# Optimization experiments

Hardware: AMD Instinct MI355X
Metric: run time of the kernel (lower is better)

## Reference

```python
import jax, jax.numpy as jnp
import numpy as np
from jax import lax

EPS = 1e-5

def _ln(x, w, b):
    m = jnp.mean(x, axis=-1, keepdims=True)
    v = jnp.mean((x - m) ** 2, axis=-1, keepdims=True)
    return (x - m) / jnp.sqrt(v + EPS) * w + b

def setup_inputs() -> dict:
    key = jax.random.key(0)
    ks = jax.random.split(key, 16)
    B, H, W, C = 4, 128, 128, 96
    N = H * W
    hidden = 192          # int(2.0 * dim)
    qk = 48               # dim // 2
    x = jax.random.normal(ks[0], (B, N, C), dtype=jnp.float32)
    # LayerNorm params
    norm_w = jnp.ones((C,), jnp.float32); norm_b = jnp.zeros((C,), jnp.float32)
    n1_w = jnp.ones((C,), jnp.float32); n1_b = jnp.zeros((C,), jnp.float32)
    n2_w = jnp.ones((C,), jnp.float32); n2_b = jnp.zeros((C,), jnp.float32)
    # Linear weights stored as [in, out]
    Wh = jax.random.normal(ks[1], (C, hidden), jnp.float32) * 0.02
    bh = jnp.zeros((hidden,), jnp.float32)
    Wqk = jax.random.normal(ks[2], (C, qk), jnp.float32) * 0.02
    bqk = jnp.zeros((qk,), jnp.float32)
    proj_w = jax.random.normal(ks[3], (C, C), jnp.float32) * 0.02
    proj_b = jnp.zeros((C,), jnp.float32)
    # per-branch affine on qk (init: normal std 0.02 / zeros, as in torch code)
    g1 = jax.random.normal(ks[4], (2, qk), jnp.float32) * 0.02
    be1 = jnp.zeros((2, qk), jnp.float32)
    g2 = jax.random.normal(ks[5], (2, qk), jnp.float32) * 0.02
    be2 = jnp.zeros((2, qk), jnp.float32)
    # SR convs (OIHW), kaiming-like init fan_out = k*k*C
    sr1_w = jax.random.normal(ks[6], (C, C, 8, 8), jnp.float32) * np.sqrt(2.0 / (8 * 8 * C))
    sr1_b = jnp.zeros((C,), jnp.float32)
    sr2_w = jax.random.normal(ks[7], (C, C, 4, 4), jnp.float32) * np.sqrt(2.0 / (4 * 4 * C))
    sr2_b = jnp.zeros((C,), jnp.float32)
    return dict(x=x, H=H, W=W, norm_w=norm_w, norm_b=norm_b, Wh=Wh, bh=bh,
                Wqk=Wqk, bqk=bqk, g1=g1, be1=be1, g2=g2, be2=be2,
                sr1_w=sr1_w, sr1_b=sr1_b, sr2_w=sr2_w, sr2_b=sr2_b,
                n1_w=n1_w, n1_b=n1_b, n2_w=n2_w, n2_b=n2_b,
                proj_w=proj_w, proj_b=proj_b)

def _sr_branch(xmap, cw, cb, lw, lb, stride):
    # xmap: [B,C,H,W]; strided conv with kernel==stride, then LN+GELU over tokens
    y = lax.conv_general_dilated(xmap, cw, (stride, stride), 'VALID',
                                 dimension_numbers=('NCHW', 'OIHW', 'NCHW'))
    y = y + cb[:, None, None]
    B, C = y.shape[0], y.shape[1]
    y = y.reshape(B, C, -1).transpose(0, 2, 1)  # [B, N', C]
    return jax.nn.gelu(_ln(y, lw, lb), approximate=False)

def reference(x, H, W, norm_w, norm_b, Wh, bh, Wqk, bqk, g1, be1, g2, be2,
              sr1_w, sr1_b, sr2_w, sr2_b, n1_w, n1_b, n2_w, n2_b, proj_w, proj_b):
    B, N, C = x.shape
    half = C // 2  # C // num_heads with num_heads=2
    nx = _ln(x, norm_w, norm_b)
    h = jax.nn.silu(nx @ Wh + bh)              # [B,N,2C]
    v, gate = h[..., :C], h[..., C:]
    xmap = nx.transpose(0, 2, 1).reshape(B, C, H, W)
    x1 = _sr_branch(xmap, sr1_w, sr1_b, n1_w, n1_b, 8)   # [B, N/64, C]
    x2 = _sr_branch(xmap, sr2_w, sr2_b, n2_w, n2_b, 4)   # [B, N/16, C]
    Z1 = jax.nn.silu(x1 @ Wqk + bqk)           # [B,N1,qk]
    QK1 = Z1[..., None, :] * g1 + be1          # [B,N1,2,qk]
    q1, k1 = QK1[..., 0, :], QK1[..., 1, :]
    Z2 = jax.nn.silu(x2 @ Wqk + bqk)
    QK2 = Z2[..., None, :] * g2 + be2
    q2, k2 = QK2[..., 0, :], QK2[..., 1, :]
    inv_n = 1.0 / N
    a1 = jnp.einsum('bnd,bmd->bnm', v[..., :half], q1) * inv_n
    A1 = jnp.square(jax.nn.relu(a1))
    V1 = jnp.einsum('bnm,bmd->bnd', A1, k1)
    a2 = jnp.einsum('bnd,bmd->bnm', v[..., half:], q2) * inv_n
    A2 = jnp.square(jax.nn.relu(a2))
    V2 = jnp.einsum('bnm,bmd->bnd', A2, k2)
    xc = jnp.concatenate([V1, V2], axis=-1)    # [B,N,C]
    value = xc * gate
    out = value @ proj_w + proj_b
    return out + xc
```

## Files before the change

kernel.cpp:

```cpp
#include <hip/hip_runtime.h>
#include <math.h>

#define NB   4
#define IH   128
#define IW   128
#define NTOK 16384
#define CC   96
#define HID  192
#define QKD  48
#define EPSF 1e-5f
#define INV_N (1.0f/16384.0f)

typedef __attribute__((ext_vector_type(8))) short sh8;
typedef __attribute__((ext_vector_type(4))) short ush4;
typedef __attribute__((ext_vector_type(4))) float f32x4;

__device__ __forceinline__ float wave_sum64(float v){
    #pragma unroll
    for (int off = 32; off > 0; off >>= 1) v += __shfl_xor(v, off, 64);
    return v;
}
__device__ __forceinline__ float siluf(float x){ return x / (1.0f + __expf(-x)); }
__device__ __forceinline__ float geluf(float x){ return 0.5f*x*(1.0f + erff(x*0.7071067811865475f)); }

__device__ __forceinline__ unsigned short f2bf(float f){
    union { float f; unsigned u; } x; x.f = f;
    unsigned u = x.u + 0x7FFFu + ((x.u >> 16) & 1u);
    return (unsigned short)(u >> 16);
}
__device__ __forceinline__ float b2f(unsigned hi16){
    union { unsigned u; float f; } c; c.u = hi16; return c.f;
}
__device__ __forceinline__ unsigned cvtpk(float a, float b){
    unsigned r;
    asm("v_cvt_pk_bf16_f32 %0, %1, %2" : "=v"(r) : "v"(a), "v"(b));
    return r;
}
__device__ __forceinline__ void swap32(unsigned &x, unsigned &y){
    asm volatile("v_permlane32_swap_b32 %0, %1" : "+v"(x), "+v"(y));
}
__device__ __forceinline__ void swap16(unsigned &x, unsigned &y){
    asm volatile("v_permlane16_swap_b32 %0, %1" : "+v"(x), "+v"(y));
}

__global__ __launch_bounds__(256) void k_ln(const float* __restrict__ x,
                                            const float* __restrict__ w,
                                            const float* __restrict__ bb,
                                            unsigned short* __restrict__ nxbf,
                                            unsigned short* __restrict__ nxim,
                                            const float* __restrict__ s1, unsigned short* __restrict__ d1, int n1,
                                            const float* __restrict__ s2, unsigned short* __restrict__ d2, int n2){
    int bid = blockIdx.x;
    if (bid >= 16384){
        int i4 = ((bid - 16384)*256 + threadIdx.x)*4;
        if (i4 < n1){
            float4 v = *(const float4*)(s1 + i4);
            unsigned u0 = cvtpk(v.x, v.y), u1 = cvtpk(v.z, v.w);
            ush4 o = {(short)u0, (short)(u0>>16), (short)u1, (short)(u1>>16)};
            *(ush4*)(d1 + i4) = o;
        } else {
            int j = i4 - n1;
            if (j < n2){
                float4 v = *(const float4*)(s2 + j);
                unsigned u0 = cvtpk(v.x, v.y), u1 = cvtpk(v.z, v.w);
                ush4 o = {(short)u0, (short)(u0>>16), (short)u1, (short)(u1>>16)};
                *(ush4*)(d2 + j) = o;
            }
        }
        return;
    }
    __shared__ unsigned short tile[4][96];
    int r = threadIdx.x >> 6;
    int row = bid*4 + r;
    int l = threadIdx.x & 63;
    const float* xr = x + (size_t)row*CC;
    float a = xr[l];
    float b = (l < 32) ? xr[64+l] : 0.0f;
    float s = wave_sum64(a + b);
    float m = s * (1.0f/96.0f);
    float d1f = a - m;
    float d2f = b - m;
    float sq = d1f*d1f + ((l < 32) ? d2f*d2f : 0.0f);
    float var = wave_sum64(sq) * (1.0f/96.0f);
    float rstd = rsqrtf(var + EPSF);
    unsigned short b1 = f2bf(d1f*rstd*w[l] + bb[l]);
    nxbf[(size_t)row*CC + l] = b1;
    tile[r][l] = b1;
    if (l < 32){
        unsigned short b2 = f2bf(d2f*rstd*w[64+l] + bb[64+l]);
        nxbf[(size_t)row*CC + 64 + l] = b2;
        tile[r][64+l] = b2;
    }
    __syncthreads();
    int t = threadIdx.x;
    if (t < 96){
        int row0 = bid*4;
        int bb2 = row0 >> 14, hw = row0 & 16383;
        ush4 v = {(short)tile[0][t], (short)tile[1][t], (short)tile[2][t], (short)tile[3][t]};
        *(ush4*)(nxim + (((size_t)(bb2*96 + t)) << 14) + hw) = v;
    }
}

__global__ __launch_bounds__(256) void k_hgemm(const unsigned short* __restrict__ nxbf,
                                               const float* __restrict__ Wh,
                                               const float* __restrict__ bh,
                                               unsigned short* __restrict__ vbuf,
                                               unsigned short* __restrict__ gate){
    __shared__ unsigned short whbf[192*100];
    int tid  = threadIdx.x;
    int lane = tid & 63;
    int wid  = tid >> 6;
    int lo   = lane & 15;
    int g    = lane >> 4;
    int row0 = blockIdx.x*64 + wid*16;

    #pragma unroll
    for (int it = 0; it < 36; it++){
        int pidx = tid + it*256;
        int k = pidx / 96, cp = (pidx - k*96)*2;
        float2 v = *(const float2*)&Wh[k*HID + cp];
        unsigned u = cvtpk(v.x, v.y);
        whbf[cp*100 + k]     = (unsigned short)u;
        whbf[(cp+1)*100 + k] = (unsigned short)(u >> 16);
    }

    sh8 a[3];
    {
        const unsigned short* ar = nxbf + (size_t)(row0 + lo)*CC;
        #pragma unroll
        for (int kc = 0; kc < 3; kc++)
            a[kc] = *(const sh8*)(ar + kc*32 + g*8);
    }
    __syncthreads();

    f32x4 acc[12];
    #pragma unroll
    for (int ct = 0; ct < 12; ct++) acc[ct] = (f32x4){0.f,0.f,0.f,0.f};
    #pragma unroll
    for (int ct = 0; ct < 12; ct++){
        #pragma unroll
        for (int kc = 0; kc < 3; kc++){
            sh8 bw = *(const sh8*)&whbf[(ct*16 + lo)*100 + kc*32 + g*8];
            acc[ct] = __builtin_amdgcn_mfma_f32_16x16x32_bf16(a[kc], bw, acc[ct], 0, 0, 0);
        }
    }

    #pragma unroll
    for (int ct = 0; ct < 12; ct++){
        int col = ct*16 + lo;
        float bcol = bh[col];
        #pragma unroll
        for (int j = 0; j < 4; j++){
            size_t row = row0 + g*4 + j;
            float hv = siluf(acc[ct][j] + bcol);
            unsigned short hb = (unsigned short)cvtpk(hv, hv);
            if (col < 96) vbuf[row*CC + col] = hb;
            else          gate[row*CC + col - 96] = hb;
        }
    }
}

__global__ __launch_bounds__(256) void k_conv(const unsigned short* __restrict__ nxim,
                                              const unsigned short* __restrict__ wbf,
                                              float* __restrict__ part,
                                              int posLog, int pdimLog, int pszLog,
                                              int kTotal, int rowblocks){
    __shared__ unsigned short pt[64*72];
    __shared__ unsigned short wt[96*72];
    int bx = blockIdx.x;
    int rb = bx % rowblocks;
    int split = bx / rowblocks;
    int tid = threadIdx.x;
    int lane = tid & 63, wid = tid >> 6, lo = lane & 15, g = lane >> 4;
    int psz = 1 << pszLog, pdim = 1 << pdimLog;
    int ksLog = 2*pszLog;
    int kb0 = split * 192;
    int cinc = (64 >> ksLog) << 14;

    int j   = tid & 15;
    int coff = (j*4) >> ksLog;
    int s   = (j*4) & (psz*psz - 1);
    int sy  = s >> pszLog, sx = s & (psz-1);
    int pAddr[4], pOff[4];
    #pragma unroll
    for (int i = 0; i < 4; i++){
        int p = (tid >> 4) + 16*i;
        int R = rb*64 + p;
        int b = R >> posLog, pp = R & ((1 << posLog) - 1);
        int pi = pp >> pdimLog, pj = pp & (pdim-1);
        pAddr[i] = (((b*96 + coff) + (kb0 >> ksLog)) << 14) + (pi*psz + sy)*IW + pj*psz + sx;
        pOff[i]  = p*72 + j*4;
    }
    int jj = tid & 7;
    int wAddr[3], wOff[3];
    #pragma unroll
    for (int i = 0; i < 3; i++){
        int o = (tid >> 3) + 32*i;
        wAddr[i] = o*kTotal + kb0 + jj*8;
        wOff[i]  = o*72 + jj*8;
    }

    f32x4 acc[6];
    #pragma unroll
    for (int ct = 0; ct < 6; ct++) acc[ct] = (f32x4){0.f,0.f,0.f,0.f};

    ush4 pr[4]; sh8 wr[3];
    #pragma unroll
    for (int i = 0; i < 4; i++) pr[i] = *(const ush4*)(nxim + pAddr[i]);
    #pragma unroll
    for (int i = 0; i < 3; i++) wr[i] = *(const sh8*)(wbf + wAddr[i]);

    for (int ch = 0; ch < 3; ch++){
        __syncthreads();
        #pragma unroll
        for (int i = 0; i < 4; i++) *(ush4*)&pt[pOff[i]] = pr[i];
        #pragma unroll
        for (int i = 0; i < 3; i++) *(sh8*)&wt[wOff[i]] = wr[i];
        if (ch < 2){
            #pragma unroll
            for (int i = 0; i < 4; i++){ pAddr[i] += cinc; pr[i] = *(const ush4*)(nxim + pAddr[i]); }
            #pragma unroll
            for (int i = 0; i < 3; i++){ wAddr[i] += 64;  wr[i] = *(const sh8*)(wbf + wAddr[i]); }
        }
        __syncthreads();

        sh8 a0 = *(const sh8*)&pt[(wid*16 + lo)*72 + g*8];
        sh8 a1 = *(const sh8*)&pt[(wid*16 + lo)*72 + 32 + g*8];
        #pragma unroll
        for (int ct = 0; ct < 6; ct++){
            sh8 b0 = *(const sh8*)&wt[(ct*16 + lo)*72 + g*8];
            sh8 b1 = *(const sh8*)&wt[(ct*16 + lo)*72 + 32 + g*8];
            acc[ct] = __builtin_amdgcn_mfma_f32_16x16x32_bf16(a0, b0, acc[ct], 0, 0, 0);
            acc[ct] = __builtin_amdgcn_mfma_f32_16x16x32_bf16(a1, b1, acc[ct], 0, 0, 0);
        }
    }

    int rowsTotal = NB << posLog;
    #pragma unroll
    for (int ct = 0; ct < 6; ct++){
        int o = ct*16 + lo;
        #pragma unroll
        for (int jx = 0; jx < 4; jx++){
            int R = rb*64 + wid*16 + g*4 + jx;
            part[((size_t)split*rowsTotal + R)*96 + o] = acc[ct][jx];
        }
    }
}

__global__ __launch_bounds__(64) void k_reduce(const float* __restrict__ part1,
                                               const float* __restrict__ part2,
                                               const float* __restrict__ cb1, const float* __restrict__ cb2,
                                               const float* __restrict__ lw1, const float* __restrict__ lw2,
                                               const float* __restrict__ lb1, const float* __restrict__ lb2,
                                               const float* __restrict__ wqk,
                                               const float* __restrict__ bqk,
                                               const float* __restrict__ g1, const float* __restrict__ g2,
                                               const float* __restrict__ be1, const float* __restrict__ be2,
                                               unsigned short* __restrict__ qp1, unsigned short* __restrict__ qp2,
                                               unsigned short* __restrict__ kt1, unsigned short* __restrict__ kt2){
    __shared__ float xsh[96];
    int bid = blockIdx.x;
    bool fst = bid < 1024;
    int row   = fst ? bid : bid - 1024;
    int nsplit= fst ? 32 : 8;
    int rows  = fst ? 1024 : 4096;
    int Mper  = fst ? 256 : 1024;
    const float* part = fst ? part1 : part2;
    const float* cbias= fst ? cb1 : cb2;
    const float* lw   = fst ? lw1 : lw2;
    const float* lb   = fst ? lb1 : lb2;
    const float* g    = fst ? g1 : g2;
    const float* be   = fst ? be1 : be2;
    unsigned short* qp = fst ? qp1 : qp2;
    unsigned short* ktp= fst ? kt1 : kt2;

    int l = threadIdx.x;
    float y1 = 0.0f, y2 = 0.0f;
    for (int s = 0; s < nsplit; s++){
        const float* pr = part + ((size_t)s*rows + row)*96;
        y1 += pr[l];
        if (l < 32) y2 += pr[64+l];
    }
    y1 += cbias[l];
    if (l < 32) y2 += cbias[64+l];
    float s = wave_sum64(y1 + ((l < 32) ? y2 : 0.0f));
    float m = s * (1.0f/96.0f);
    float d1 = y1 - m, d2 = y2 - m;
    float var = wave_sum64(d1*d1 + ((l < 32) ? d2*d2 : 0.0f)) * (1.0f/96.0f);
    float rstd = rsqrtf(var + EPSF);
    xsh[l] = geluf(d1*rstd*lw[l] + lb[l]);
    if (l < 32) xsh[64+l] = geluf(d2*rstd*lw[64+l] + lb[64+l]);
    __syncthreads();
    if (l < 48){
        float z = bqk[l];
        #pragma unroll 4
        for (int c = 0; c < 96; c++) z += xsh[c]*wqk[c*48 + l];
        z = siluf(z);
        float qv = (z*g[l]    + be[l]) * INV_N;
        float kv =  z*g[48+l] + be[48+l];
        int b = row / Mper, p = row - b*Mper;
        qp[(size_t)row*64 + l] = f2bf(qv);
        ktp[((size_t)b*48 + l)*Mper + p] = f2bf(kv);
    } else {
        qp[(size_t)row*64 + l] = 0;
    }
}

__global__ __launch_bounds__(256) void k_attn(const unsigned short* __restrict__ vbuf,
                                              const unsigned short* __restrict__ qp1,
                                              const unsigned short* __restrict__ ktp1,
                                              const unsigned short* __restrict__ qp2,
                                              const unsigned short* __restrict__ ktp2,
                                              unsigned short* __restrict__ V1,
                                              unsigned short* __restrict__ V2){
    __shared__ unsigned short qs[2][32*72];
    __shared__ unsigned short ks[2][48*72];

    int bx   = blockIdx.x;
    int kind = (bx < 512) ? 1 : 0;
    int blk  = (bx < 512) ? bx : bx - 512;
    int tid  = threadIdx.x;
    int wid  = tid >> 6;
    int lane = tid & 63;
    int lo   = lane & 15;
    int g    = lane >> 4;
    int row0 = blk*128 + wid*32;
    int b    = row0 >> 14;

    int   M    = kind ? 1024 : 256;
    const unsigned short* qp = (kind ? qp2 : qp1) + (size_t)b*M*64;
    const unsigned short* kt = (kind ? ktp2 : ktp1) + (size_t)b*48*M;
    int   voff = kind ? 48 : 0;
    unsigned short* vout = kind ? V2 : V1;

    sh8 vb[2][2];
    #pragma unroll
    for (int nt = 0; nt < 2; nt++){
        const unsigned short* vrow = vbuf + (size_t)(row0 + nt*16 + lo)*CC + voff;
        vb[nt][0] = *(const sh8*)(vrow + g*8);
        if (g < 2) vb[nt][1] = *(const sh8*)(vrow + 32 + g*8);
        else { sh8 z = {0,0,0,0,0,0,0,0}; vb[nt][1] = z; }
    }

    int qm = tid >> 3, qj = tid & 7;
    int kd = tid >> 2, kj = tid & 3;
    bool kact = tid < 192;

    f32x4 acc[2][3];
    #pragma unroll
    for (int nt = 0; nt < 2; nt++)
        #pragma unroll
        for (int dt = 0; dt < 3; dt++) acc[nt][dt] = (f32x4){0.f,0.f,0.f,0.f};

    int nchunk = M >> 5;
    sh8 qreg = *(const sh8*)(qp + (size_t)qm*64 + qj*8);
    sh8 kreg;
    if (kact) kreg = *(const sh8*)(kt + (size_t)kd*M + kj*8);

    for (int ch = 0; ch < nchunk; ch++){
        int bs = ch & 1;
        unsigned short* qb = qs[bs];
        unsigned short* kb = ks[bs];
        *(sh8*)&qb[qm*72 + qj*8] = qreg;
        if (kact) *(sh8*)&kb[kd*72 + kj*8] = kreg;
        __syncthreads();
        if (ch + 1 < nchunk){
            int mb2 = (ch + 1)*32;
            qreg = *(const sh8*)(qp + (size_t)(mb2 + qm)*64 + qj*8);
            if (kact) kreg = *(const sh8*)(kt + (size_t)kd*M + mb2 + kj*8);
        }

        sh8 aq[2][2];
        #pragma unroll
        for (int mt = 0; mt < 2; mt++)
            #pragma unroll
            for (int kc = 0; kc < 2; kc++)
                aq[mt][kc] = *(const sh8*)&qb[(mt*16 + lo)*72 + kc*32 + g*8];
        f32x4 c00, c01, c10, c11;
        c00 = (f32x4){0.f,0.f,0.f,0.f}; c01 = c00; c10 = c00; c11 = c00;
        c00 = __builtin_amdgcn_mfma_f32_16x16x32_bf16(aq[0][0], vb[0][0], c00, 0,0,0);
        c00 = __builtin_amdgcn_mfma_f32_16x16x32_bf16(aq[0][1], vb[0][1], c00, 0,0,0);
        c01 = __builtin_amdgcn_mfma_f32_16x16x32_bf16(aq[0][0], vb[1][0], c01, 0,0,0);
        c01 = __builtin_amdgcn_mfma_f32_16x16x32_bf16(aq[0][1], vb[1][1], c01, 0,0,0);
        c10 = __builtin_amdgcn_mfma_f32_16x16x32_bf16(aq[1][0], vb[0][0], c10, 0,0,0);
        c10 = __builtin_amdgcn_mfma_f32_16x16x32_bf16(aq[1][1], vb[0][1], c10, 0,0,0);
        c11 = __builtin_amdgcn_mfma_f32_16x16x32_bf16(aq[1][0], vb[1][0], c11, 0,0,0);
        c11 = __builtin_amdgcn_mfma_f32_16x16x32_bf16(aq[1][1], vb[1][1], c11, 0,0,0);

        sh8 pa[2];
        #pragma unroll
        for (int nt = 0; nt < 2; nt++){
            f32x4 cm0 = nt ? c01 : c00;
            f32x4 cm1 = nt ? c11 : c10;
            float p00 = fmaxf(cm0[0], 0.f); p00 *= p00;
            float p01 = fmaxf(cm0[1], 0.f); p01 *= p01;
            float p02 = fmaxf(cm0[2], 0.f); p02 *= p02;
            float p03 = fmaxf(cm0[3], 0.f); p03 *= p03;
            float p10 = fmaxf(cm1[0], 0.f); p10 *= p10;
            float p11 = fmaxf(cm1[1], 0.f); p11 *= p11;
            float p12 = fmaxf(cm1[2], 0.f); p12 *= p12;
            float p13 = fmaxf(cm1[3], 0.f); p13 *= p13;
            unsigned a0 = cvtpk(p00, p01);
            unsigned a1 = cvtpk(p02, p03);
            unsigned b0 = cvtpk(p10, p11);
            unsigned b1 = cvtpk(p12, p13);
            swap32(a0, b0); swap16(a0, b0);
            swap32(a1, b1); swap16(a1, b1);
            union { unsigned u[4]; sh8 v; } pk;
            pk.u[0] = a0; pk.u[1] = a1; pk.u[2] = b0; pk.u[3] = b1;
            pa[nt] = pk.v;
        }

        #pragma unroll
        for (int dt = 0; dt < 3; dt++){
            sh8 bk = *(const sh8*)&kb[(dt*16 + lo)*72 + g*8];
            acc[0][dt] = __builtin_amdgcn_mfma_f32_16x16x32_bf16(pa[0], bk, acc[0][dt], 0, 0, 0);
            acc[1][dt] = __builtin_amdgcn_mfma_f32_16x16x32_bf16(pa[1], bk, acc[1][dt], 0, 0, 0);
        }
    }

    #pragma unroll
    for (int nt = 0; nt < 2; nt++)
        #pragma unroll
        for (int dt = 0; dt < 3; dt++)
            #pragma unroll
            for (int j = 0; j < 4; j++)
                vout[(size_t)(row0 + nt*16 + g*4 + j)*48 + dt*16 + lo] =
                    (unsigned short)cvtpk(acc[nt][dt][j], acc[nt][dt][j]);
}

__global__ __launch_bounds__(256) void k_final(const unsigned short* __restrict__ V1,
                                               const unsigned short* __restrict__ V2,
                                               const unsigned short* __restrict__ gate,
                                               const float* __restrict__ projw,
                                               const float* __restrict__ projb,
                                               float* __restrict__ out){
    __shared__ unsigned short pjbf[96*100];
    int tid  = threadIdx.x;
    int lane = tid & 63;
    int wid  = tid >> 6;
    int lo   = lane & 15;
    int g    = lane >> 4;
    int row0 = blockIdx.x*64 + wid*16;

    #pragma unroll
    for (int it = 0; it < 18; it++){
        int pidx = tid + it*256;
        int k = pidx / 48, cp = (pidx - k*48)*2;
        float2 v = *(const float2*)&projw[k*CC + cp];
        unsigned u = cvtpk(v.x, v.y);
        pjbf[cp*100 + k]     = (unsigned short)u;
        pjbf[(cp+1)*100 + k] = (unsigned short)(u >> 16);
    }

    sh8 a[3];
    {
        size_t row = row0 + lo;
        const unsigned short* gr = gate + row*CC;
        #pragma unroll
        for (int kc = 0; kc < 3; kc++){
            int d0 = kc*32 + g*8;
            const unsigned short* xsrc = (d0 < 48) ? (V1 + row*48 + d0) : (V2 + row*48 + d0 - 48);
            union { sh8 v; unsigned u[4]; } xu, gu, pk;
            xu.v = *(const sh8*)xsrc;
            gu.v = *(const sh8*)(gr + d0);
            #pragma unroll
            for (int i = 0; i < 4; i++){
                float xl = b2f(xu.u[i] << 16),        xh = b2f(xu.u[i] & 0xffff0000u);
                float gl = b2f(gu.u[i] << 16),        gh = b2f(gu.u[i] & 0xffff0000u);
                pk.u[i] = cvtpk(xl*gl, xh*gh);
            }
            a[kc] = pk.v;
        }
    }
    __syncthreads();

    f32x4 acc[6];
    #pragma unroll
    for (int ct = 0; ct < 6; ct++) acc[ct] = (f32x4){0.f,0.f,0.f,0.f};
    #pragma unroll
    for (int ct = 0; ct < 6; ct++){
        #pragma unroll
        for (int kc = 0; kc < 3; kc++){
            sh8 bw = *(const sh8*)&pjbf[(ct*16 + lo)*100 + kc*32 + g*8];
            acc[ct] = __builtin_amdgcn_mfma_f32_16x16x32_bf16(a[kc], bw, acc[ct], 0, 0, 0);
        }
    }

    #pragma unroll
    for (int ct = 0; ct < 6; ct++){
        int col = ct*16 + lo;
        float bcol = projb[col];
        const unsigned short* xsrc = (ct < 3) ? (V1 + col) : (V2 + col - 48);
        #pragma unroll
        for (int j = 0; j < 4; j++){
            size_t row = row0 + g*4 + j;
            float xc = b2f((unsigned)xsrc[row*48] << 16);
            out[row*CC + col] = acc[ct][j] + bcol + xc;
        }
    }
}

extern "C" void kernel_launch(void* const* d_in, const int* in_sizes, int n_in,
                              void* d_out, int out_size, void* d_ws, size_t ws_size,
                              hipStream_t stream){
    const float* x      = (const float*)d_in[0];
    const float* norm_w = (const float*)d_in[3];
    const float* norm_b = (const float*)d_in[4];
    const float* Wh     = (const float*)d_in[5];
    const float* bh     = (const float*)d_in[6];
    const float* Wqk    = (const float*)d_in[7];
    const float* bqk    = (const float*)d_in[8];
    const float* g1     = (const float*)d_in[9];
    const float* be1    = (const float*)d_in[10];
    const float* g2     = (const float*)d_in[11];
    const float* be2    = (const float*)d_in[12];
    const float* sr1_w  = (const float*)d_in[13];
    const float* sr1_b  = (const float*)d_in[14];
    const float* sr2_w  = (const float*)d_in[15];
    const float* sr2_b  = (const float*)d_in[16];
    const float* n1_w   = (const float*)d_in[17];
    const float* n1_b   = (const float*)d_in[18];
    const float* n2_w   = (const float*)d_in[19];
    const float* n2_b   = (const float*)d_in[20];
    const float* proj_w = (const float*)d_in[21];
    const float* proj_b = (const float*)d_in[22];
    float* out = (float*)d_out;

    float* ws = (float*)d_ws;
    size_t off = 0;
    unsigned short* nxbf = (unsigned short*)(ws + off); off += (size_t)NB*NTOK*CC/2;
    unsigned short* nxim = (unsigned short*)(ws + off); off += (size_t)NB*NTOK*CC/2;
    unsigned short* w1bf = (unsigned short*)(ws + off); off += (size_t)96*6144/2;
    unsigned short* w2bf = (unsigned short*)(ws + off); off += (size_t)96*1536/2;
    unsigned short* vbuf = (unsigned short*)(ws + off); off += (size_t)NB*NTOK*CC/2;
    unsigned short* gate = (unsigned short*)(ws + off); off += (size_t)NB*NTOK*CC/2;
    unsigned short* qp1 = (unsigned short*)(ws + off); off += (size_t)NB*256*64/2;
    unsigned short* kt1 = (unsigned short*)(ws + off); off += (size_t)NB*48*256/2;
    unsigned short* qp2 = (unsigned short*)(ws + off); off += (size_t)NB*1024*64/2;
    unsigned short* kt2 = (unsigned short*)(ws + off); off += (size_t)NB*48*1024/2;
    float* part1= ws + off; off += (size_t)32*NB*256*96;
    float* part2= ws + off; off += (size_t)8*NB*1024*96;
    unsigned short* V1 = (unsigned short*)(ws + off); off += (size_t)NB*NTOK*48/2;
    unsigned short* V2 = (unsigned short*)(ws + off); off += (size_t)NB*NTOK*48/2;
    if (ws_size < off*sizeof(float)) return;

    k_ln   <<<17104, 256, 0, stream>>>(x, norm_w, norm_b, nxbf, nxim,
                                       sr1_w, w1bf, 96*6144, sr2_w, w2bf, 96*1536);
    k_hgemm<<<1024, 256, 0, stream>>>(nxbf, Wh, bh, vbuf, gate);
    k_conv <<<512, 256, 0, stream>>>(nxim, w1bf, part1, 8, 4, 3, 6144, 16);
    k_conv <<<512, 256, 0, stream>>>(nxim, w2bf, part2, 10, 5, 2, 1536, 64);
    k_reduce<<<5120, 64, 0, stream>>>(part1, part2, sr1_b, sr2_b, n1_w, n2_w, n1_b, n2_b,
                                      Wqk, bqk, g1, g2, be1, be2, qp1, qp2, kt1, kt2);
    k_attn <<<1024, 256, 0, stream>>>(vbuf, qp1, kt1, qp2, kt2, V1, V2);
    k_final<<<1024, 256, 0, stream>>>(V1, V2, gate, proj_w, proj_b, out);
}
```

Before: 122.0 us.

## Merge hgemm and both SR convs into one launch; halve conv split-K; widen attention tiles

Combines the hidden-projection GEMM and the two strided-conv GEMMs into a single kernel that dispatches on block index, so the three independent stages share one launch and fill the GPU together. Each conv block now covers 384 reduction elements instead of 192, which halves the split-K partial buffers and the reduce work at the cost of fewer conv blocks. The attention kernel moves to 128-thread blocks where each wave handles 64 rows, reusing every Q/K tile loaded into LDS across more MFMAs but raising register pressure.

```diff
diff --git a/kernel.cpp b/kernel.cpp
--- a/kernel.cpp
+++ b/kernel.cpp
@@ -101,18 +101,116 @@
     }
 }
 
-__global__ __launch_bounds__(256) void k_hgemm(const unsigned short* __restrict__ nxbf,
-                                               const float* __restrict__ Wh,
-                                               const float* __restrict__ bh,
-                                               unsigned short* __restrict__ vbuf,
-                                               unsigned short* __restrict__ gate){
-    __shared__ unsigned short whbf[192*100];
+__device__ __forceinline__ void conv_body(const unsigned short* __restrict__ nxim,
+                                          const unsigned short* __restrict__ wbf,
+                                          float* __restrict__ part,
+                                          int posLog, int pdimLog, int pszLog,
+                                          int kTotal, int rb, int split,
+                                          unsigned short* pt, unsigned short* wt){
+    const int NCH = 6;
+    int tid = threadIdx.x;
+    int lane = tid & 63, wid = tid >> 6, lo = lane & 15, g = lane >> 4;
+    int psz = 1 << pszLog, pdim = 1 << pdimLog;
+    int ksLog = 2*pszLog;
+    int kb0 = split * 384;
+    int cinc = (64 >> ksLog) << 14;
+
+    int j   = tid & 15;
+    int coff = (j*4) >> ksLog;
+    int s   = (j*4) & (psz*psz - 1);
+    int sy  = s >> pszLog, sx = s & (psz-1);
+    int pAddr[4], pOff[4];
+    #pragma unroll
+    for (int i = 0; i < 4; i++){
+        int p = (tid >> 4) + 16*i;
+        int R = rb*64 + p;
+        int b = R >> posLog, pp = R & ((1 << posLog) - 1);
+        int pi = pp >> pdimLog, pj = pp & (pdim-1);
+        pAddr[i] = (((b*96 + coff) + (kb0 >> ksLog)) << 14) + (pi*psz + sy)*IW + pj*psz + sx;
+        pOff[i]  = p*72 + j*4;
+    }
+    int jj = tid & 7;
+    int wAddr[3], wOff[3];
+    #pragma unroll
+    for (int i = 0; i < 3; i++){
+        int o = (tid >> 3) + 32*i;
+        wAddr[i] = o*kTotal + kb0 + jj*8;
+        wOff[i]  = o*72 + jj*8;
+    }
+
+    f32x4 acc[6];
+    #pragma unroll
+    for (int ct = 0; ct < 6; ct++) acc[ct] = (f32x4){0.f,0.f,0.f,0.f};
+
+    ush4 pr[4]; sh8 wr[3];
+    #pragma unroll
+    for (int i = 0; i < 4; i++) pr[i] = *(const ush4*)(nxim + pAddr[i]);
+    #pragma unroll
+    for (int i = 0; i < 3; i++) wr[i] = *(const sh8*)(wbf + wAddr[i]);
+
+    for (int ch = 0; ch < NCH; ch++){
+        __syncthreads();
+        #pragma unroll
+        for (int i = 0; i < 4; i++) *(ush4*)&pt[pOff[i]] = pr[i];
+        #pragma unroll
+        for (int i = 0; i < 3; i++) *(sh8*)&wt[wOff[i]] = wr[i];
+        if (ch < NCH-1){
+            #pragma unroll
+            for (int i = 0; i < 4; i++){ pAddr[i] += cinc; pr[i] = *(const ush4*)(nxim + pAddr[i]); }
+            #pragma unroll
+            for (int i = 0; i < 3; i++){ wAddr[i] += 64;  wr[i] = *(const sh8*)(wbf + wAddr[i]); }
+        }
+        __syncthreads();
+
+        sh8 a0 = *(const sh8*)&pt[(wid*16 + lo)*72 + g*8];
+        sh8 a1 = *(const sh8*)&pt[(wid*16 + lo)*72 + 32 + g*8];
+        #pragma unroll
+        for (int ct = 0; ct < 6; ct++){
+            sh8 b0 = *(const sh8*)&wt[(ct*16 + lo)*72 + g*8];
+            sh8 b1 = *(const sh8*)&wt[(ct*16 + lo)*72 + 32 + g*8];
+            acc[ct] = __builtin_amdgcn_mfma_f32_16x16x32_bf16(a0, b0, acc[ct], 0, 0, 0);
+            acc[ct] = __builtin_amdgcn_mfma_f32_16x16x32_bf16(a1, b1, acc[ct], 0, 0, 0);
+        }
+    }
+
+    int rowsTotal = NB << posLog;
+    #pragma unroll
+    for (int ct = 0; ct < 6; ct++){
+        int o = ct*16 + lo;
+        #pragma unroll
+        for (int jx = 0; jx < 4; jx++){
+            int R = rb*64 + wid*16 + g*4 + jx;
+            part[((size_t)split*rowsTotal + R)*96 + o] = acc[ct][jx];
+        }
+    }
+}
+
+__global__ __launch_bounds__(256) void k_mid(const unsigned short* __restrict__ nxbf,
+                                             const unsigned short* __restrict__ nxim,
+                                             const float* __restrict__ Wh,
+                                             const float* __restrict__ bh,
+                                             const unsigned short* __restrict__ w1bf,
+                                             const unsigned short* __restrict__ w2bf,
+                                             unsigned short* __restrict__ vbuf,
+                                             unsigned short* __restrict__ gate,
+                                             float* __restrict__ part1,
+                                             float* __restrict__ part2){
+    __shared__ unsigned short smem[192*100];
+    int bid = blockIdx.x;
+    if (bid < 512){
+        unsigned short* pt = smem;
+        unsigned short* wt = smem + 64*72;
+        if (bid < 256) conv_body(nxim, w1bf, part1, 8, 4, 3, 6144, bid & 15, bid >> 4, pt, wt);
+        else { int b2 = bid - 256; conv_body(nxim, w2bf, part2, 10, 5, 2, 1536, b2 & 63, b2 >> 6, pt, wt); }
+        return;
+    }
+    unsigned short* whbf = smem;
     int tid  = threadIdx.x;
     int lane = tid & 63;
     int wid  = tid >> 6;
     int lo   = lane & 15;
     int g    = lane >> 4;
-    int row0 = blockIdx.x*64 + wid*16;
+    int row0 = (bid - 512)*64 + wid*16;
 
     #pragma unroll
     for (int it = 0; it < 36; it++){
@@ -156,93 +254,6 @@
             unsigned short hb = (unsigned short)cvtpk(hv, hv);
             if (col < 96) vbuf[row*CC + col] = hb;
             else          gate[row*CC + col - 96] = hb;
-        }
-    }
-}
-
-__global__ __launch_bounds__(256) void k_conv(const unsigned short* __restrict__ nxim,
-                                              const unsigned short* __restrict__ wbf,
-                                              float* __restrict__ part,
-                                              int posLog, int pdimLog, int pszLog,
-                                              int kTotal, int rowblocks){
-    __shared__ unsigned short pt[64*72];
-    __shared__ unsigned short wt[96*72];
-    int bx = blockIdx.x;
-    int rb = bx % rowblocks;
-    int split = bx / rowblocks;
-    int tid = threadIdx.x;
-    int lane = tid & 63, wid = tid >> 6, lo = lane & 15, g = lane >> 4;
-    int psz = 1 << pszLog, pdim = 1 << pdimLog;
-    int ksLog = 2*pszLog;
-    int kb0 = split * 192;
-    int cinc = (64 >> ksLog) << 14;
-
-    int j   = tid & 15;
-    int coff = (j*4) >> ksLog;
-    int s   = (j*4) & (psz*psz - 1);
-    int sy  = s >> pszLog, sx = s & (psz-1);
-    int pAddr[4], pOff[4];
-    #pragma unroll
-    for (int i = 0; i < 4; i++){
-        int p = (tid >> 4) + 16*i;
-        int R = rb*64 + p;
-        int b = R >> posLog, pp = R & ((1 << posLog) - 1);
-        int pi = pp >> pdimLog, pj = pp & (pdim-1);
-        pAddr[i] = (((b*96 + coff) + (kb0 >> ksLog)) << 14) + (pi*psz + sy)*IW + pj*psz + sx;
-        pOff[i]  = p*72 + j*4;
-    }
-    int jj = tid & 7;
-    int wAddr[3], wOff[3];
-    #pragma unroll
-    for (int i = 0; i < 3; i++){
-        int o = (tid >> 3) + 32*i;
-        wAddr[i] = o*kTotal + kb0 + jj*8;
-        wOff[i]  = o*72 + jj*8;
-    }
-
-    f32x4 acc[6];
-    #pragma unroll
-    for (int ct = 0; ct < 6; ct++) acc[ct] = (f32x4){0.f,0.f,0.f,0.f};
-
-    ush4 pr[4]; sh8 wr[3];
-    #pragma unroll
-    for (int i = 0; i < 4; i++) pr[i] = *(const ush4*)(nxim + pAddr[i]);
-    #pragma unroll
-    for (int i = 0; i < 3; i++) wr[i] = *(const sh8*)(wbf + wAddr[i]);
-
-    for (int ch = 0; ch < 3; ch++){
-        __syncthreads();
-        #pragma unroll
-        for (int i = 0; i < 4; i++) *(ush4*)&pt[pOff[i]] = pr[i];
-        #pragma unroll
-        for (int i = 0; i < 3; i++) *(sh8*)&wt[wOff[i]] = wr[i];
-        if (ch < 2){
-            #pragma unroll
-            for (int i = 0; i < 4; i++){ pAddr[i] += cinc; pr[i] = *(const ush4*)(nxim + pAddr[i]); }
-            #pragma unroll
-            for (int i = 0; i < 3; i++){ wAddr[i] += 64;  wr[i] = *(const sh8*)(wbf + wAddr[i]); }
-        }
-        __syncthreads();
-
-        sh8 a0 = *(const sh8*)&pt[(wid*16 + lo)*72 + g*8];
-        sh8 a1 = *(const sh8*)&pt[(wid*16 + lo)*72 + 32 + g*8];
-        #pragma unroll
-        for (int ct = 0; ct < 6; ct++){
-            sh8 b0 = *(const sh8*)&wt[(ct*16 + lo)*72 + g*8];
-            sh8 b1 = *(const sh8*)&wt[(ct*16 + lo)*72 + 32 + g*8];
-            acc[ct] = __builtin_amdgcn_mfma_f32_16x16x32_bf16(a0, b0, acc[ct], 0, 0, 0);
-            acc[ct] = __builtin_amdgcn_mfma_f32_16x16x32_bf16(a1, b1, acc[ct], 0, 0, 0);
-        }
-    }
-
-    int rowsTotal = NB << posLog;
-    #pragma unroll
-    for (int ct = 0; ct < 6; ct++){
-        int o = ct*16 + lo;
-        #pragma unroll
-        for (int jx = 0; jx < 4; jx++){
-            int R = rb*64 + wid*16 + g*4 + jx;
-            part[((size_t)split*rowsTotal + R)*96 + o] = acc[ct][jx];
         }
     }
 }
@@ -262,7 +273,7 @@
     int bid = blockIdx.x;
     bool fst = bid < 1024;
     int row   = fst ? bid : bid - 1024;
-    int nsplit= fst ? 32 : 8;
+    int nsplit= fst ? 16 : 4;
     int rows  = fst ? 1024 : 4096;
     int Mper  = fst ? 256 : 1024;
     const float* part = fst ? part1 : part2;
@@ -306,7 +317,7 @@
     }
 }
 
-__global__ __launch_bounds__(256) void k_attn(const unsigned short* __restrict__ vbuf,
+__global__ __launch_bounds__(128) void k_attn(const unsigned short* __restrict__ vbuf,
                                               const unsigned short* __restrict__ qp1,
                                               const unsigned short* __restrict__ ktp1,
                                               const unsigned short* __restrict__ qp2,
@@ -324,7 +335,7 @@
     int lane = tid & 63;
     int lo   = lane & 15;
     int g    = lane >> 4;
-    int row0 = blk*128 + wid*32;
+    int row0 = blk*128 + wid*64;
     int b    = row0 >> 14;
 
     int   M    = kind ? 1024 : 256;
@@ -333,41 +344,47 @@
     int   voff = kind ? 48 : 0;
     unsigned short* vout = kind ? V2 : V1;
 
-    sh8 vb[2][2];
-    #pragma unroll
-    for (int nt = 0; nt < 2; nt++){
+    sh8 vb[4][2];
+    #pragma unroll
+    for (int nt = 0; nt < 4; nt++){
         const unsigned short* vrow = vbuf + (size_t)(row0 + nt*16 + lo)*CC + voff;
         vb[nt][0] = *(const sh8*)(vrow + g*8);
         if (g < 2) vb[nt][1] = *(const sh8*)(vrow + 32 + g*8);
         else { sh8 z = {0,0,0,0,0,0,0,0}; vb[nt][1] = z; }
     }
 
-    int qm = tid >> 3, qj = tid & 7;
-    int kd = tid >> 2, kj = tid & 3;
-    bool kact = tid < 192;
-
-    f32x4 acc[2][3];
-    #pragma unroll
-    for (int nt = 0; nt < 2; nt++)
+    int q0r = tid >> 3, q0c = tid & 7;
+    int k0d = tid >> 2, k0m = tid & 3;
+    bool k2 = tid < 64;
+
+    f32x4 acc[4][3];
+    #pragma unroll
+    for (int nt = 0; nt < 4; nt++)
         #pragma unroll
         for (int dt = 0; dt < 3; dt++) acc[nt][dt] = (f32x4){0.f,0.f,0.f,0.f};
 
     int nchunk = M >> 5;
-    sh8 qreg = *(const sh8*)(qp + (size_t)qm*64 + qj*8);
-    sh8 kreg;
-    if (kact) kreg = *(const sh8*)(kt + (size_t)kd*M + kj*8);
+    sh8 qr0 = *(const sh8*)(qp + (size_t)q0r*64 + q0c*8);
+    sh8 qr1 = *(const sh8*)(qp + (size_t)(16 + q0r)*64 + q0c*8);
+    sh8 kr0 = *(const sh8*)(kt + (size_t)k0d*M + k0m*8);
+    sh8 kr1;
+    if (k2) kr1 = *(const sh8*)(kt + (size_t)(32 + k0d)*M + k0m*8);
 
     for (int ch = 0; ch < nchunk; ch++){
         int bs = ch & 1;
         unsigned short* qb = qs[bs];
         unsigned short* kb = ks[bs];
-        *(sh8*)&qb[qm*72 + qj*8] = qreg;
-        if (kact) *(sh8*)&kb[kd*72 + kj*8] = kreg;
+        *(sh8*)&qb[q0r*72 + q0c*8] = qr0;
+        *(sh8*)&qb[(16 + q0r)*72 + q0c*8] = qr1;
+        *(sh8*)&kb[k0d*72 + k0m*8] = kr0;
+        if (k2) *(sh8*)&kb[(32 + k0d)*72 + k0m*8] = kr1;
         __syncthreads();
         if (ch + 1 < nchunk){
             int mb2 = (ch + 1)*32;
-            qreg = *(const sh8*)(qp + (size_t)(mb2 + qm)*64 + qj*8);
-            if (kact) kreg = *(const sh8*)(kt + (size_t)kd*M + mb2 + kj*8);
+            qr0 = *(const sh8*)(qp + (size_t)(mb2 + q0r)*64 + q0c*8);
+            qr1 = *(const sh8*)(qp + (size_t)(mb2 + 16 + q0r)*64 + q0c*8);
+            kr0 = *(const sh8*)(kt + (size_t)k0d*M + mb2 + k0m*8);
+            if (k2) kr1 = *(const sh8*)(kt + (size_t)(32 + k0d)*M + mb2 + k0m*8);
         }
 
         sh8 aq[2][2];
@@ -376,22 +393,22 @@
             #pragma unroll
             for (int kc = 0; kc < 2; kc++)
                 aq[mt][kc] = *(const sh8*)&qb[(mt*16 + lo)*72 + kc*32 + g*8];
-        f32x4 c00, c01, c10, c11;
-        c00 = (f32x4){0.f,0.f,0.f,0.f}; c01 = c00; c10 = c00; c11 = c00;
-        c00 = __builtin_amdgcn_mfma_f32_16x16x32_bf16(aq[0][0], vb[0][0], c00, 0,0,0);
-        c00 = __builtin_amdgcn_mfma_f32_16x16x32_bf16(aq[0][1], vb[0][1], c00, 0,0,0);
-        c01 = __builtin_amdgcn_mfma_f32_16x16x32_bf16(aq[0][0], vb[1][0], c01, 0,0,0);
-        c01 = __builtin_amdgcn_mfma_f32_16x16x32_bf16(aq[0][1], vb[1][1], c01, 0,0,0);
-        c10 = __builtin_amdgcn_mfma_f32_16x16x32_bf16(aq[1][0], vb[0][0], c10, 0,0,0);
-        c10 = __builtin_amdgcn_mfma_f32_16x16x32_bf16(aq[1][1], vb[0][1], c10, 0,0,0);
-        c11 = __builtin_amdgcn_mfma_f32_16x16x32_bf16(aq[1][0], vb[1][0], c11, 0,0,0);
-        c11 = __builtin_amdgcn_mfma_f32_16x16x32_bf16(aq[1][1], vb[1][1], c11, 0,0,0);
-
-        sh8 pa[2];
-        #pragma unroll
-        for (int nt = 0; nt < 2; nt++){
-            f32x4 cm0 = nt ? c01 : c00;
-            f32x4 cm1 = nt ? c11 : c10;
+        f32x4 c[2][4];
+        #pragma unroll
+        for (int mt = 0; mt < 2; mt++)
+            #pragma unroll
+            for (int nt = 0; nt < 4; nt++){
+                f32x4 cc = (f32x4){0.f,0.f,0.f,0.f};
+                cc = __builtin_amdgcn_mfma_f32_16x16x32_bf16(aq[mt][0], vb[nt][0], cc, 0,0,0);
+                cc = __builtin_amdgcn_mfma_f32_16x16x32_bf16(aq[mt][1], vb[nt][1], cc, 0,0,0);
+                c[mt][nt] = cc;
+            }
+
+        sh8 pa[4];
+        #pragma unroll
+        for (int nt = 0; nt < 4; nt++){
+            f32x4 cm0 = c[0][nt];
+            f32x4 cm1 = c[1][nt];
             float p00 = fmaxf(cm0[0], 0.f); p00 *= p00;
             float p01 = fmaxf(cm0[1], 0.f); p01 *= p01;
             float p02 = fmaxf(cm0[2], 0.f); p02 *= p02;
@@ -414,13 +431,14 @@
         #pragma unroll
         for (int dt = 0; dt < 3; dt++){
             sh8 bk = *(const sh8*)&kb[(dt*16 + lo)*72 + g*8];
-            acc[0][dt] = __builtin_amdgcn_mfma_f32_16x16x32_bf16(pa[0], bk, acc[0][dt], 0, 0, 0);
-            acc[1][dt] = __builtin_amdgcn_mfma_f32_16x16x32_bf16(pa[1], bk, acc[1][dt], 0, 0, 0);
-        }
-    }
-
-    #pragma unroll
-    for (int nt = 0; nt < 2; nt++)
+            #pragma unroll
+            for (int nt = 0; nt < 4; nt++)
+                acc[nt][dt] = __builtin_amdgcn_mfma_f32_16x16x32_bf16(pa[nt], bk, acc[nt][dt], 0, 0, 0);
+        }
+    }
+
+    #pragma unroll
+    for (int nt = 0; nt < 4; nt++)
         #pragma unroll
         for (int dt = 0; dt < 3; dt++)
             #pragma unroll
@@ -539,19 +557,17 @@
     unsigned short* kt1 = (unsigned short*)(ws + off); off += (size_t)NB*48*256/2;
     unsigned short* qp2 = (unsigned short*)(ws + off); off += (size_t)NB*1024*64/2;
     unsigned short* kt2 = (unsigned short*)(ws + off); off += (size_t)NB*48*1024/2;
-    float* part1= ws + off; off += (size_t)32*NB*256*96;
-    float* part2= ws + off; off += (size_t)8*NB*1024*96;
+    float* part1= ws + off; off += (size_t)16*NB*256*96;
+    float* part2= ws + off; off += (size_t)4*NB*1024*96;
     unsigned short* V1 = (unsigned short*)(ws + off); off += (size_t)NB*NTOK*48/2;
     unsigned short* V2 = (unsigned short*)(ws + off); off += (size_t)NB*NTOK*48/2;
     if (ws_size < off*sizeof(float)) return;
 
     k_ln   <<<17104, 256, 0, stream>>>(x, norm_w, norm_b, nxbf, nxim,
                                        sr1_w, w1bf, 96*6144, sr2_w, w2bf, 96*1536);
-    k_hgemm<<<1024, 256, 0, stream>>>(nxbf, Wh, bh, vbuf, gate);
-    k_conv <<<512, 256, 0, stream>>>(nxim, w1bf, part1, 8, 4, 3, 6144, 16);
-    k_conv <<<512, 256, 0, stream>>>(nxim, w2bf, part2, 10, 5, 2, 1536, 64);
+    k_mid  <<<1536, 256, 0, stream>>>(nxbf, nxim, Wh, bh, w1bf, w2bf, vbuf, gate, part1, part2);
     k_reduce<<<5120, 64, 0, stream>>>(part1, part2, sr1_b, sr2_b, n1_w, n2_w, n1_b, n2_b,
                                       Wqk, bqk, g1, g2, be1, be2, qp1, qp2, kt1, kt2);
-    k_attn <<<1024, 256, 0, stream>>>(vbuf, qp1, kt1, qp2, kt2, V1, V2);
+    k_attn <<<1024, 128, 0, stream>>>(vbuf, qp1, kt1, qp2, kt2, V1, V2);
     k_final<<<1024, 256, 0, stream>>>(V1, V2, gate, proj_w, proj_b, out);
 }
```

Result: slower. 134.1 us (+9.9%).
